# Performance work log

Hardware: AMD Instinct MI355X
Metric: run time of the kernel (lower is better)

The kernel has to match this reference:

```python
import jax, jax.numpy as jnp
import numpy as np

N_NODES = 100000
N_EDGES = 1600000
IN_DIM, FEAT_DIM, HID_DIM, OUT_DIM = 256, 128, 128, 128


def _glorot(key, shape):
    lim = float(np.sqrt(6.0 / (shape[0] + shape[1])))
    return jax.random.uniform(key, shape, jnp.float32, -lim, lim)


def setup_inputs() -> dict:
    key = jax.random.key(0)
    ks = jax.random.split(key, 6)
    x = jax.random.normal(ks[0], (N_NODES, IN_DIM), jnp.float32)
    edge_index = jax.random.randint(ks[1], (2, N_EDGES), 0, N_NODES, dtype=jnp.int64)
    return {
        "x": x,
        "edge_index": edge_index,
        "Wp": _glorot(ks[2], (IN_DIM, FEAT_DIM)),
        "bp": jnp.zeros((FEAT_DIM,), jnp.float32),
        "W1": _glorot(ks[3], (FEAT_DIM, HID_DIM)),
        "b1": jnp.zeros((HID_DIM,), jnp.float32),
        "W2": _glorot(ks[4], (HID_DIM, OUT_DIM)),
        "b2": jnp.zeros((OUT_DIM,), jnp.float32),
    }


def _gcn_conv(h, W, b, src, dst, norm, deg_inv, n):
    # PyG GCNConv: linear first, symmetric-normalized aggregation (with
    # self-loops), bias after aggregation. Self-loop term = z_i / deg_i.
    z = h @ W                                   # [N, out]
    msg = (norm[src] * norm[dst])[:, None] * z[src]  # [E, out]
    agg = jax.ops.segment_sum(msg, dst, num_segments=n)
    return agg + z * deg_inv[:, None] + b


def reference(x, edge_index, Wp, bp, W1, b1, W2, b2):
    src, dst = edge_index[0], edge_index[1]
    n = x.shape[0]
    # degrees on A + I (self-loop adds 1)
    deg = jax.ops.segment_sum(jnp.ones(src.shape[0], x.dtype), dst, num_segments=n) + 1.0
    norm = jax.lax.rsqrt(deg)
    deg_inv = 1.0 / deg
    h = x @ Wp + bp                              # feature_pre linear
    h = jax.nn.relu(_gcn_conv(h, W1, b1, src, dst, norm, deg_inv, n))
    # dropout is identity in eval mode; layer_num=2 -> no hidden convs
    return _gcn_conv(h, W2, b2, src, dst, norm, deg_inv, n)
```

## Files before the change

### kernel.cpp

```cpp
#include <hip/hip_runtime.h>
#include <cstdint>
#include <cstddef>

#define N_NODES 100000
#define N_EDGES 1600000

constexpr int NPB = 512;
constexpr int NBUCK = (N_NODES + NPB - 1) / NPB;
constexpr int EPB = 8192;
constexpr int NCHUNK = (N_EDGES + EPB - 1) / EPB;

typedef _Float16 half8 __attribute__((ext_vector_type(8)));
typedef _Float16 half2v __attribute__((ext_vector_type(2)));
typedef float f32x4 __attribute__((ext_vector_type(4)));

__global__ __launch_bounds__(256) void b1_hist(const int* __restrict__ dst,
                                               int* __restrict__ bbc) {
    __shared__ int hist[NBUCK];
    int t = threadIdx.x;
    if (t < NBUCK) hist[t] = 0;
    __syncthreads();
    int base = blockIdx.x * EPB;
#pragma unroll
    for (int i = 0; i < EPB / 256; ++i) {
        int e = base + i * 256 + t;
        if (e < N_EDGES) atomicAdd(&hist[dst[e] >> 9], 1);
    }
    __syncthreads();
    if (t < NBUCK) bbc[t * NCHUNK + blockIdx.x] = hist[t];
}

__global__ void b_scan(int* __restrict__ bbc, int* __restrict__ bucketOff,
                       int* __restrict__ rowStart) {
    __shared__ int tot[NBUCK];
    int t = threadIdx.x;
    if (t < NBUCK) {
        int run = 0;
        for (int blk = 0; blk < NCHUNK; ++blk) {
            int idx = t * NCHUNK + blk;
            int c = bbc[idx];
            bbc[idx] = run;
            run += c;
        }
        tot[t] = run;
    }
    __syncthreads();
    if (t == 0) {
        int acc = 0;
        for (int b = 0; b < NBUCK; ++b) {
            bucketOff[b] = acc;
            acc += tot[b];
        }
        bucketOff[NBUCK] = acc;
        rowStart[N_NODES] = acc;
    }
}

__global__ __launch_bounds__(256) void b2_scatter(const int* __restrict__ src,
                                                  const int* __restrict__ dst,
                                                  const int* __restrict__ bbc,
                                                  const int* __restrict__ bucketOff,
                                                  int* __restrict__ staged) {
    __shared__ int cnt[NBUCK];
    __shared__ int base[NBUCK];
    int t = threadIdx.x;
    if (t < NBUCK) {
        cnt[t] = 0;
        base[t] = bucketOff[t] + bbc[t * NCHUNK + blockIdx.x];
    }
    __syncthreads();
    int ebase = blockIdx.x * EPB;
#pragma unroll
    for (int i = 0; i < EPB / 256; ++i) {
        int e = ebase + i * 256 + t;
        if (e < N_EDGES) {
            int d = dst[e];
            int b = d >> 9;
            int r = atomicAdd(&cnt[b], 1);
            staged[base[b] + r] = ((d & 511) << 17) | src[e];
        }
    }
}

__global__ __launch_bounds__(256) void b3_sort(const int* __restrict__ staged,
                                               const int* __restrict__ bucketOff,
                                               int* __restrict__ rowStart,
                                               float* __restrict__ normv,
                                               int* __restrict__ colIdx) {
    __shared__ int hist[NPB];
    __shared__ int sc0[NPB], sc1[NPB];
    __shared__ int cursor[NPB];
    int t = threadIdx.x;
    int b = blockIdx.x;
    int e0 = bucketOff[b], e1 = bucketOff[b + 1];
    int ne = e1 - e0;
    int node0 = b * NPB;
    int nn = min(NPB, N_NODES - node0);

    for (int j = t; j < NPB; j += 256) hist[j] = 0;
    __syncthreads();
    for (int idx = t; idx < ne; idx += 256)
        atomicAdd(&hist[staged[e0 + idx] >> 17], 1);
    __syncthreads();
    for (int j = t; j < NPB; j += 256) sc0[j] = hist[j];
    __syncthreads();
    int* s = sc0;
    int* d = sc1;
    for (int off = 1; off < NPB; off <<= 1) {
        for (int j = t; j < NPB; j += 256) d[j] = s[j] + (j >= off ? s[j - off] : 0);
        __syncthreads();
        int* tmp = s; s = d; d = tmp;
    }
    for (int j = t; j < NPB; j += 256) {
        int excl = s[j] - hist[j];
        cursor[j] = excl;
        if (j < nn) {
            rowStart[node0 + j] = e0 + excl;
            normv[node0 + j] = (float)(1.0 / sqrt((double)(hist[j] + 1)));
        }
    }
    __syncthreads();
    for (int idx = t; idx < ne; idx += 256) {
        int v = staged[e0 + idx];
        int dl = v >> 17;
        int sn = v & 0x1FFFF;
        int r = atomicAdd(&cursor[dl], 1);
        colIdx[e0 + r] = sn;
    }
}

__global__ void wc_kernel(const float* __restrict__ Wp, const float* __restrict__ bp,
                          const float* __restrict__ W1, float* __restrict__ Wc,
                          float* __restrict__ bc) {
    int r = blockIdx.x;
    int cc = threadIdx.x;
    float acc = 0.f;
    if (r < 256) {
        for (int k = 0; k < 128; ++k) acc = fmaf(Wp[r * 128 + k], W1[k * 128 + cc], acc);
        Wc[r * 128 + cc] = acc;
    } else {
        for (int k = 0; k < 128; ++k) acc = fmaf(bp[k], W1[k * 128 + cc], acc);
        bc[cc] = acc;
    }
}

__global__ void tsplit_kernel(const float* __restrict__ W, _Float16* __restrict__ Oh,
                              _Float16* __restrict__ Ol, int K) {
    int id = blockIdx.x * 256 + threadIdx.x;
    if (id >= K * 128) return;
    int n = id / K;
    int k = id - n * K;
    float v = W[k * 128 + n];
    _Float16 h = (_Float16)v;
    Oh[id] = h;
    Ol[id] = (_Float16)(v - (float)h);
}

template <bool AF16, int K>
__global__ __launch_bounds__(1024) void mfma_gemm_p(
    const float* __restrict__ Af, const _Float16* __restrict__ Ah,
    const _Float16* __restrict__ Bth, const _Float16* __restrict__ Btl,
    const float* __restrict__ bias, const float* __restrict__ scale,
    _Float16* __restrict__ Ch, int M, int nstrip) {
    constexpr int NSLAB = K / 32;
    constexpr int JROW = K / 8;
    __shared__ _Float16 sBh[128 * K];
    __shared__ _Float16 sBl[128 * K];

    const int t = threadIdx.x;
    for (int idx = t; idx < 128 * JROW; idx += 1024) {
        int n = idx / JROW;
        int j = idx - n * JROW;
        int d = n * K + (((j & 7) ^ (n & 7)) << 3) + ((j >> 3) << 6);
        *(half8*)&sBh[d] = *(const half8*)(Bth + n * K + (j << 3));
        *(half8*)&sBl[d] = *(const half8*)(Btl + n * K + (j << 3));
    }
    __syncthreads();

    const int lane = t & 63;
    const int q = lane >> 4;
    const int mr = lane & 15;
    const int mre = mr & 7;
    const int gw = (blockIdx.x << 4) + (t >> 6);
    const int wstride = gridDim.x << 4;

    for (int strip = gw; strip < nstrip; strip += wstride) {
        const int row0 = strip * 16;
        int ar = row0 + mr;
        if (ar >= M) ar = M - 1;

        f32x4 acc[8];
#pragma unroll
        for (int nt = 0; nt < 8; ++nt) acc[nt] = (f32x4){0.f, 0.f, 0.f, 0.f};

        f32x4 pf[2][2];
        half8 ph[2];

#define LOAD_SLAB(SLOT, SS)                                                    \
        {                                                                      \
            if constexpr (AF16) {                                              \
                ph[SLOT] = *(const half8*)(Ah + (size_t)ar * K + (SS) * 32 + q * 8); \
            } else {                                                           \
                const float* ap = Af + (size_t)ar * K + (SS) * 32 + q * 8;     \
                pf[SLOT][0] = *(const f32x4*)ap;                               \
                pf[SLOT][1] = *(const f32x4*)(ap + 4);                         \
            }                                                                  \
        }

        LOAD_SLAB(0, 0)
        LOAD_SLAB(1, 1)

#pragma unroll
        for (int s = 0; s < NSLAB; ++s) {
            const int sl = s & 1;
            half8 ah, al;
            if constexpr (AF16) {
                ah = ph[sl];
            } else {
                f32x4 a0 = pf[sl][0];
                f32x4 a1 = pf[sl][1];
#pragma unroll
                for (int jj = 0; jj < 4; ++jj) {
                    _Float16 h0 = (_Float16)a0[jj];
                    _Float16 h1 = (_Float16)a1[jj];
                    ah[jj] = h0;
                    ah[jj + 4] = h1;
                    al[jj] = (_Float16)(a0[jj] - (float)h0);
                    al[jj + 4] = (_Float16)(a1[jj] - (float)h1);
                }
            }
            if (s + 2 < NSLAB) LOAD_SLAB(sl, s + 2)

            const int kof = ((s >> 1) << 6) + ((((s & 1) << 2) | q) ^ mre) * 8;
#pragma unroll
            for (int nt = 0; nt < 8; ++nt) {
                const int bo = (nt * 16 + mr) * K + kof;
                half8 bh = *(const half8*)&sBh[bo];
                half8 bl = *(const half8*)&sBl[bo];
                acc[nt] = __builtin_amdgcn_mfma_f32_16x16x32_f16(ah, bh, acc[nt], 0, 0, 0);
                acc[nt] = __builtin_amdgcn_mfma_f32_16x16x32_f16(ah, bl, acc[nt], 0, 0, 0);
                if constexpr (!AF16)
                    acc[nt] = __builtin_amdgcn_mfma_f32_16x16x32_f16(al, bh, acc[nt], 0, 0, 0);
            }
            __builtin_amdgcn_sched_barrier(0x38F);
        }
#undef LOAD_SLAB

#pragma unroll
        for (int rr = 0; rr < 4; ++rr) {
            int row = row0 + q * 4 + rr;
            if (row >= M) continue;
            float sc = scale[row];
#pragma unroll
            for (int nt = 0; nt < 8; ++nt) {
                float bv = bias ? bias[nt * 16 + mr] : 0.f;
                Ch[(size_t)row * 128 + nt * 16 + mr] =
                    (_Float16)((acc[nt][rr] + bv) * sc);
            }
        }
    }
}

__global__ __launch_bounds__(256) void agg_kernel(const _Float16* __restrict__ zs,
                                                  const int* __restrict__ rowStart,
                                                  const int* __restrict__ colIdx,
                                                  const float* __restrict__ normv,
                                                  const float* __restrict__ bias,
                                                  float* __restrict__ outF,
                                                  _Float16* __restrict__ outH,
                                                  int doRelu) {
    int wid = (blockIdx.x * 256 + threadIdx.x) >> 6;
    int lane = threadIdx.x & 63;
    if (wid >= N_NODES) return;
    int s0 = rowStart[wid];
    int s1 = rowStart[wid + 1];
    const int c = lane * 2;
    const _Float16* zc = zs + c;

    float2 a0 = make_float2(0.f, 0.f), a1 = a0, a2 = a0, a3 = a0;
    int e = s0;
    for (; e + 8 <= s1; e += 8) {
        int i0 = colIdx[e + 0], i1 = colIdx[e + 1], i2 = colIdx[e + 2], i3 = colIdx[e + 3];
        int i4 = colIdx[e + 4], i5 = colIdx[e + 5], i6 = colIdx[e + 6], i7 = colIdx[e + 7];
        half2v v0 = *(const half2v*)(zc + (size_t)i0 * 128);
        half2v v1 = *(const half2v*)(zc + (size_t)i1 * 128);
        half2v v2 = *(const half2v*)(zc + (size_t)i2 * 128);
        half2v v3 = *(const half2v*)(zc + (size_t)i3 * 128);
        half2v v4 = *(const half2v*)(zc + (size_t)i4 * 128);
        half2v v5 = *(const half2v*)(zc + (size_t)i5 * 128);
        half2v v6 = *(const half2v*)(zc + (size_t)i6 * 128);
        half2v v7 = *(const half2v*)(zc + (size_t)i7 * 128);
        a0.x += (float)v0[0] + (float)v4[0]; a0.y += (float)v0[1] + (float)v4[1];
        a1.x += (float)v1[0] + (float)v5[0]; a1.y += (float)v1[1] + (float)v5[1];
        a2.x += (float)v2[0] + (float)v6[0]; a2.y += (float)v2[1] + (float)v6[1];
        a3.x += (float)v3[0] + (float)v7[0]; a3.y += (float)v3[1] + (float)v7[1];
    }
    if (e + 4 <= s1) {
        int i0 = colIdx[e + 0], i1 = colIdx[e + 1], i2 = colIdx[e + 2], i3 = colIdx[e + 3];
        half2v v0 = *(const half2v*)(zc + (size_t)i0 * 128);
        half2v v1 = *(const half2v*)(zc + (size_t)i1 * 128);
        half2v v2 = *(const half2v*)(zc + (size_t)i2 * 128);
        half2v v3 = *(const half2v*)(zc + (size_t)i3 * 128);
        a0.x += (float)v0[0]; a0.y += (float)v0[1];
        a1.x += (float)v1[0]; a1.y += (float)v1[1];
        a2.x += (float)v2[0]; a2.y += (float)v2[1];
        a3.x += (float)v3[0]; a3.y += (float)v3[1];
        e += 4;
    }
    for (; e < s1; ++e) {
        int i0 = colIdx[e];
        half2v v0 = *(const half2v*)(zc + (size_t)i0 * 128);
        a0.x += (float)v0[0]; a0.y += (float)v0[1];
    }

    half2v self = *(const half2v*)(zc + (size_t)wid * 128);
    float sx = (a0.x + a1.x) + (a2.x + a3.x) + (float)self[0];
    float sy = (a0.y + a1.y) + (a2.y + a3.y) + (float)self[1];
    float nd = normv[wid];
    float2 bv = *(const float2*)(bias + c);
    float ox = fmaf(nd, sx, bv.x);
    float oy = fmaf(nd, sy, bv.y);
    if (doRelu) {
        ox = fmaxf(ox, 0.f);
        oy = fmaxf(oy, 0.f);
    }
    if (outH) {
        half2v o;
        o[0] = (_Float16)ox;
        o[1] = (_Float16)oy;
        *(half2v*)(outH + (size_t)wid * 128 + c) = o;
    } else {
        *(float2*)(outF + (size_t)wid * 128 + c) = make_float2(ox, oy);
    }
}

extern "C" void kernel_launch(void* const* d_in, const int* in_sizes, int n_in,
                              void* d_out, int out_size, void* d_ws, size_t ws_size,
                              hipStream_t stream) {
    const float* x  = (const float*)d_in[0];
    const int* ei   = (const int*)d_in[1];
    const float* Wp = (const float*)d_in[2];
    const float* bp = (const float*)d_in[3];
    const float* W1 = (const float*)d_in[4];
    const float* b1 = (const float*)d_in[5];
    const float* W2 = (const float*)d_in[6];
    const float* b2 = (const float*)d_in[7];
    float* out = (float*)d_out;

    const int* srcIdx = ei;
    const int* dstIdx = ei + N_EDGES;

    size_t off = 0;
    auto alloc = [&](size_t bytes) -> void* {
        void* p = (char*)d_ws + off;
        off += (bytes + 511) & ~(size_t)511;
        return p;
    };
    int* rowStart   = (int*)alloc((size_t)(N_NODES + 1) * 4);
    int* colIdx     = (int*)alloc((size_t)N_EDGES * 4);
    int* staged     = (int*)alloc((size_t)N_EDGES * 4);
    int* bbc        = (int*)alloc((size_t)NBUCK * NCHUNK * 4);
    int* bucketOff  = (int*)alloc((size_t)(NBUCK + 1) * 4);
    float* normv    = (float*)alloc((size_t)N_NODES * 4);
    float* Wc       = (float*)alloc((size_t)256 * 128 * 4);
    float* bc       = (float*)alloc((size_t)128 * 4);
    _Float16* Wcth  = (_Float16*)alloc((size_t)128 * 256 * 2);
    _Float16* Wctl  = (_Float16*)alloc((size_t)128 * 256 * 2);
    _Float16* W2th  = (_Float16*)alloc((size_t)128 * 128 * 2);
    _Float16* W2tl  = (_Float16*)alloc((size_t)128 * 128 * 2);
    _Float16* zA    = (_Float16*)alloc((size_t)N_NODES * 128 * 2);
    _Float16* zB    = (_Float16*)alloc((size_t)N_NODES * 128 * 2);

    const int AB = (N_NODES + 3) / 4;
    constexpr int NSTRIP = (N_NODES + 15) / 16;

    b1_hist<<<NCHUNK, 256, 0, stream>>>(dstIdx, bbc);
    b_scan<<<1, 256, 0, stream>>>(bbc, bucketOff, rowStart);
    b2_scatter<<<NCHUNK, 256, 0, stream>>>(srcIdx, dstIdx, bbc, bucketOff, staged);
    b3_sort<<<NBUCK, 256, 0, stream>>>(staged, bucketOff, rowStart, normv, colIdx);

    wc_kernel<<<257, 128, 0, stream>>>(Wp, bp, W1, Wc, bc);
    tsplit_kernel<<<(256 * 128 + 255) / 256, 256, 0, stream>>>(Wc, Wcth, Wctl, 256);
    tsplit_kernel<<<(128 * 128 + 255) / 256, 256, 0, stream>>>(W2, W2th, W2tl, 128);

    mfma_gemm_p<false, 256><<<256, 1024, 0, stream>>>(x, nullptr, Wcth, Wctl, bc, normv,
                                                      zA, N_NODES, NSTRIP);
    agg_kernel<<<AB, 256, 0, stream>>>(zA, rowStart, colIdx, normv, b1, nullptr, zB, 1);
    mfma_gemm_p<true, 128><<<256, 1024, 0, stream>>>(nullptr, zB, W2th, W2tl, nullptr, normv,
                                                     zA, N_NODES, NSTRIP);
    agg_kernel<<<AB, 256, 0, stream>>>(zA, rowStart, colIdx, normv, b2, out, nullptr, 0);
}
```

Measured before the change: 437.7 us.

## Store features in 16-column slices and aggregate per slice for gather locality

The intermediate fp16 feature matrices switch from row-major [N,128] to eight column slices of [N,16]. The GEMM writes and reads that layout, and aggregation runs one grid pass per slice, so each slice (about 3.2 MB) can stay resident in cache while it is gathered randomly. Within a wavefront, 8 edge groups each load one 32-byte slice row and the partial sums are combined with cross-lane shuffles. This adds 8x more blocks, and each slice re-reads rowStart and colIdx, in exchange for a smaller random-gather working set.

```diff
diff --git a/kernel.cpp b/kernel.cpp
--- a/kernel.cpp
+++ b/kernel.cpp
@@ -9,6 +9,7 @@
 constexpr int NBUCK = (N_NODES + NPB - 1) / NPB;
 constexpr int EPB = 8192;
 constexpr int NCHUNK = (N_EDGES + EPB - 1) / EPB;
+constexpr int AGB = (N_NODES + 3) / 4;
 
 typedef _Float16 half8 __attribute__((ext_vector_type(8)));
 typedef _Float16 half2v __attribute__((ext_vector_type(2)));
@@ -199,7 +200,9 @@
 #define LOAD_SLAB(SLOT, SS)                                                    \
         {                                                                      \
             if constexpr (AF16) {                                              \
-                ph[SLOT] = *(const half8*)(Ah + (size_t)ar * K + (SS) * 32 + q * 8); \
+                const int ko = (SS) * 32 + q * 8;                              \
+                ph[SLOT] = *(const half8*)(Ah +                                \
+                    ((size_t)(ko >> 4) * M + ar) * 16 + (ko & 15));            \
             } else {                                                           \
                 const float* ap = Af + (size_t)ar * K + (SS) * 32 + q * 8;     \
                 pf[SLOT][0] = *(const f32x4*)ap;                               \
@@ -254,83 +257,76 @@
 #pragma unroll
             for (int nt = 0; nt < 8; ++nt) {
                 float bv = bias ? bias[nt * 16 + mr] : 0.f;
-                Ch[(size_t)row * 128 + nt * 16 + mr] =
+                Ch[((size_t)nt * M + row) * 16 + mr] =
                     (_Float16)((acc[nt][rr] + bv) * sc);
             }
         }
     }
 }
 
-__global__ __launch_bounds__(256) void agg_kernel(const _Float16* __restrict__ zs,
-                                                  const int* __restrict__ rowStart,
-                                                  const int* __restrict__ colIdx,
-                                                  const float* __restrict__ normv,
-                                                  const float* __restrict__ bias,
-                                                  float* __restrict__ outF,
-                                                  _Float16* __restrict__ outH,
-                                                  int doRelu) {
-    int wid = (blockIdx.x * 256 + threadIdx.x) >> 6;
+__global__ __launch_bounds__(256) void agg_slice(const _Float16* __restrict__ zs,
+                                                 const int* __restrict__ rowStart,
+                                                 const int* __restrict__ colIdx,
+                                                 const float* __restrict__ normv,
+                                                 const float* __restrict__ bias,
+                                                 float* __restrict__ outF,
+                                                 _Float16* __restrict__ outH,
+                                                 int doRelu) {
+    int blk = blockIdx.x;
+    int s = blk / AGB;
+    int chunk = blk - s * AGB;
+    int wid = chunk * 4 + (threadIdx.x >> 6);
+    if (wid >= N_NODES) return;
     int lane = threadIdx.x & 63;
-    if (wid >= N_NODES) return;
+    int eg = lane >> 3;
+    int cp = lane & 7;
+    const _Float16* zsl = zs + (size_t)s * ((size_t)N_NODES * 16) + cp * 2;
+
     int s0 = rowStart[wid];
     int s1 = rowStart[wid + 1];
-    const int c = lane * 2;
-    const _Float16* zc = zs + c;
-
-    float2 a0 = make_float2(0.f, 0.f), a1 = a0, a2 = a0, a3 = a0;
-    int e = s0;
-    for (; e + 8 <= s1; e += 8) {
-        int i0 = colIdx[e + 0], i1 = colIdx[e + 1], i2 = colIdx[e + 2], i3 = colIdx[e + 3];
-        int i4 = colIdx[e + 4], i5 = colIdx[e + 5], i6 = colIdx[e + 6], i7 = colIdx[e + 7];
-        half2v v0 = *(const half2v*)(zc + (size_t)i0 * 128);
-        half2v v1 = *(const half2v*)(zc + (size_t)i1 * 128);
-        half2v v2 = *(const half2v*)(zc + (size_t)i2 * 128);
-        half2v v3 = *(const half2v*)(zc + (size_t)i3 * 128);
-        half2v v4 = *(const half2v*)(zc + (size_t)i4 * 128);
-        half2v v5 = *(const half2v*)(zc + (size_t)i5 * 128);
-        half2v v6 = *(const half2v*)(zc + (size_t)i6 * 128);
-        half2v v7 = *(const half2v*)(zc + (size_t)i7 * 128);
-        a0.x += (float)v0[0] + (float)v4[0]; a0.y += (float)v0[1] + (float)v4[1];
-        a1.x += (float)v1[0] + (float)v5[0]; a1.y += (float)v1[1] + (float)v5[1];
-        a2.x += (float)v2[0] + (float)v6[0]; a2.y += (float)v2[1] + (float)v6[1];
-        a3.x += (float)v3[0] + (float)v7[0]; a3.y += (float)v3[1] + (float)v7[1];
-    }
-    if (e + 4 <= s1) {
-        int i0 = colIdx[e + 0], i1 = colIdx[e + 1], i2 = colIdx[e + 2], i3 = colIdx[e + 3];
-        half2v v0 = *(const half2v*)(zc + (size_t)i0 * 128);
-        half2v v1 = *(const half2v*)(zc + (size_t)i1 * 128);
-        half2v v2 = *(const half2v*)(zc + (size_t)i2 * 128);
-        half2v v3 = *(const half2v*)(zc + (size_t)i3 * 128);
-        a0.x += (float)v0[0]; a0.y += (float)v0[1];
-        a1.x += (float)v1[0]; a1.y += (float)v1[1];
-        a2.x += (float)v2[0]; a2.y += (float)v2[1];
-        a3.x += (float)v3[0]; a3.y += (float)v3[1];
-        e += 4;
-    }
-    for (; e < s1; ++e) {
+
+    float ax0 = 0.f, ay0 = 0.f, ax1 = 0.f, ay1 = 0.f;
+    int e = s0 + eg;
+    for (; e + 8 < s1; e += 16) {
         int i0 = colIdx[e];
-        half2v v0 = *(const half2v*)(zc + (size_t)i0 * 128);
-        a0.x += (float)v0[0]; a0.y += (float)v0[1];
-    }
-
-    half2v self = *(const half2v*)(zc + (size_t)wid * 128);
-    float sx = (a0.x + a1.x) + (a2.x + a3.x) + (float)self[0];
-    float sy = (a0.y + a1.y) + (a2.y + a3.y) + (float)self[1];
+        int i1 = colIdx[e + 8];
+        half2v v0 = *(const half2v*)(zsl + (size_t)i0 * 16);
+        half2v v1 = *(const half2v*)(zsl + (size_t)i1 * 16);
+        ax0 += (float)v0[0]; ay0 += (float)v0[1];
+        ax1 += (float)v1[0]; ay1 += (float)v1[1];
+    }
+    if (e < s1) {
+        int i0 = colIdx[e];
+        half2v v0 = *(const half2v*)(zsl + (size_t)i0 * 16);
+        ax0 += (float)v0[0]; ay0 += (float)v0[1];
+    }
+    float ax = ax0 + ax1, ay = ay0 + ay1;
+
+#pragma unroll
+    for (int m = 8; m < 64; m <<= 1) {
+        ax += __shfl_xor(ax, m, 64);
+        ay += __shfl_xor(ay, m, 64);
+    }
+
+    half2v sv = *(const half2v*)(zsl + (size_t)wid * 16);
     float nd = normv[wid];
+    int c = s * 16 + cp * 2;
     float2 bv = *(const float2*)(bias + c);
-    float ox = fmaf(nd, sx, bv.x);
-    float oy = fmaf(nd, sy, bv.y);
+    float ox = fmaf(nd, ax + (float)sv[0], bv.x);
+    float oy = fmaf(nd, ay + (float)sv[1], bv.y);
     if (doRelu) {
         ox = fmaxf(ox, 0.f);
         oy = fmaxf(oy, 0.f);
     }
-    if (outH) {
-        half2v o;
-        o[0] = (_Float16)ox;
-        o[1] = (_Float16)oy;
-        *(half2v*)(outH + (size_t)wid * 128 + c) = o;
-    } else {
-        *(float2*)(outF + (size_t)wid * 128 + c) = make_float2(ox, oy);
+    if (eg == 0) {
+        if (outH) {
+            half2v o;
+            o[0] = (_Float16)ox;
+            o[1] = (_Float16)oy;
+            *(half2v*)(outH + ((size_t)s * N_NODES + wid) * 16 + cp * 2) = o;
+        } else {
+            *(float2*)(outF + (size_t)wid * 128 + c) = make_float2(ox, oy);
+        }
     }
 }
 
@@ -371,7 +367,6 @@
     _Float16* zA    = (_Float16*)alloc((size_t)N_NODES * 128 * 2);
     _Float16* zB    = (_Float16*)alloc((size_t)N_NODES * 128 * 2);
 
-    const int AB = (N_NODES + 3) / 4;
     constexpr int NSTRIP = (N_NODES + 15) / 16;
 
     b1_hist<<<NCHUNK, 256, 0, stream>>>(dstIdx, bbc);
@@ -385,8 +380,10 @@
 
     mfma_gemm_p<false, 256><<<256, 1024, 0, stream>>>(x, nullptr, Wcth, Wctl, bc, normv,
                                                       zA, N_NODES, NSTRIP);
-    agg_kernel<<<AB, 256, 0, stream>>>(zA, rowStart, colIdx, normv, b1, nullptr, zB, 1);
+    agg_slice<<<8 * AGB, 256, 0, stream>>>(zA, rowStart, colIdx, normv, b1,
+                                           nullptr, zB, 1);
     mfma_gemm_p<true, 128><<<256, 1024, 0, stream>>>(nullptr, zB, W2th, W2tl, nullptr, normv,
                                                      zA, N_NODES, NSTRIP);
-    agg_kernel<<<AB, 256, 0, stream>>>(zA, rowStart, colIdx, normv, b2, out, nullptr, 0);
-}
+    agg_slice<<<8 * AGB, 256, 0, stream>>>(zA, rowStart, colIdx, normv, b2,
+                                           out, nullptr, 0);
+}
```

Measured after the change: 783.0 us. 78.9% more time.
